# Kernel optimization log

Hardware: AMD Instinct MI355X
Metric: run time of the kernel (lower is better)

## Reference

```python
import jax, jax.numpy as jnp
import numpy as np

D_MODEL = 2048
N_HEADS = 16
HEAD_DIM = D_MODEL // N_HEADS
B, T = 2, 2048


def setup_inputs() -> dict:
    key = jax.random.key(0)
    ks = jax.random.split(key, 7)
    s = 0.02
    return {
        "x": jax.random.normal(ks[0], (B, T, D_MODEL), dtype=jnp.float32),
        "w_qkv": jax.random.normal(ks[1], (D_MODEL, 3 * D_MODEL), dtype=jnp.float32) * s,
        "w_proj": jax.random.normal(ks[2], (D_MODEL, D_MODEL), dtype=jnp.float32) * s,
        "w_ff1": jax.random.normal(ks[3], (D_MODEL, 4 * D_MODEL), dtype=jnp.float32) * s,
        "b_ff1": jnp.zeros((4 * D_MODEL,), dtype=jnp.float32),
        "w_ff2": jax.random.normal(ks[4], (4 * D_MODEL, D_MODEL), dtype=jnp.float32) * s,
        "b_ff2": jnp.zeros((D_MODEL,), dtype=jnp.float32),
    }


def reference(x, w_qkv, w_proj, w_ff1, b_ff1, w_ff2, b_ff2):
    Bs, Ts, C = x.shape
    H, hd = N_HEADS, HEAD_DIM
    # fused qkv projection
    qkv = jnp.einsum("btc,cd->btd", x, w_qkv)
    q, k, v = jnp.split(qkv, 3, axis=-1)
    # (B, T, C) -> (B, H, T, hd)
    q = q.reshape(Bs, Ts, H, hd).transpose(0, 2, 1, 3)
    k = k.reshape(Bs, Ts, H, hd).transpose(0, 2, 1, 3)
    v = v.reshape(Bs, Ts, H, hd).transpose(0, 2, 1, 3)
    # paged KV write + gather round-trip (empty cache, n_kv_head == n_heads)
    # is the identity on k, v; attention is causal SDPA over the full cache.
    scale = 1.0 / jnp.sqrt(jnp.asarray(hd, dtype=x.dtype))
    scores = jnp.einsum("bhqd,bhkd->bhqk", q, k) * scale
    causal = jnp.tril(jnp.ones((Ts, Ts), dtype=bool))
    scores = jnp.where(causal, scores, jnp.finfo(scores.dtype).min)
    attn = jax.nn.softmax(scores, axis=-1)
    out = jnp.einsum("bhqk,bhkd->bhqd", attn, v)  # (B, H, T, hd)
    out = out.transpose(0, 2, 1, 3).reshape(Bs, Ts, C)
    attn_out = jnp.einsum("btc,cd->btd", out, w_proj)
    # feed-forward with exact GELU (torch nn.GELU default)
    h = jax.nn.gelu(jnp.einsum("btc,cf->btf", x, w_ff1) + b_ff1, approximate=False)
    ff_out = jnp.einsum("btf,fc->btc", h, w_ff2) + b_ff2
    return x + attn_out + ff_out
```

## Files before the change

### kernel.cpp

```cpp
#include <hip/hip_runtime.h>
#include <hip/hip_bf16.h>
#include <cmath>

typedef __bf16 bf16x8 __attribute__((ext_vector_type(8)));
typedef float f32x4 __attribute__((ext_vector_type(4)));
typedef unsigned short u16;
typedef unsigned int u32;

#define DEV __device__ __forceinline__

static constexpr int BB = 2;
static constexpr int T = 2048;
static constexpr int DM = 2048;
static constexpr int NH = 16;
static constexpr int HD = 128;
static constexpr int FF = 8192;
static constexpr int M = BB * T;
static constexpr int NQKV = 3 * DM;

DEV u16 f2b(float f) {
  u32 u = __builtin_bit_cast(u32, f);
  u = (u + 0x7FFFu + ((u >> 16) & 1u)) >> 16;
  return (u16)u;
}
DEV float b2f(u16 h) {
  u32 u = ((u32)h) << 16;
  return __builtin_bit_cast(float, u);
}

DEV void gload16(const u16* g, const u16* l) {
  __builtin_amdgcn_global_load_lds(
      (const __attribute__((address_space(1))) void*)(uintptr_t)g,
      (__attribute__((address_space(3))) void*)(unsigned)(uintptr_t)l,
      16, 0, 0);
}


__global__ void cvt_f32_to_bf16(const float* __restrict__ in, u16* __restrict__ out, int n4) {
  int i = blockIdx.x * blockDim.x + threadIdx.x;
  if (i >= n4) return;
  float4 v = reinterpret_cast<const float4*>(in)[i];
  ushort4 o;
  o.x = f2b(v.x); o.y = f2b(v.y); o.z = f2b(v.z); o.w = f2b(v.w);
  reinterpret_cast<ushort4*>(out)[i] = o;
}

__global__ void transpose_cvt(const float* __restrict__ W, u16* __restrict__ Wt, int K, int N) {
  __shared__ float tile[32][33];
  int nb = blockIdx.x * 32, kb = blockIdx.y * 32;
  int r = threadIdx.x >> 3;
  int c4 = (threadIdx.x & 7) * 4;
  float4 v = *reinterpret_cast<const float4*>(&W[(size_t)(kb + r) * N + nb + c4]);
  tile[r][c4] = v.x; tile[r][c4 + 1] = v.y; tile[r][c4 + 2] = v.z; tile[r][c4 + 3] = v.w;
  __syncthreads();
  ushort4 o;
  o.x = f2b(tile[c4][r]);     o.y = f2b(tile[c4 + 1][r]);
  o.z = f2b(tile[c4 + 2][r]); o.w = f2b(tile[c4 + 3][r]);
  *reinterpret_cast<ushort4*>(&Wt[(size_t)(nb + r) * K + kb + c4]) = o;
}

template <int EPI>
__global__ __launch_bounds__(512, 2) void gemm8(
    const u16* __restrict__ A, const u16* __restrict__ Bt, int Ndim, int K, int gx,
    u16* __restrict__ out_bf, const float* __restrict__ bias) {
  __shared__ __align__(16) u16 lds[2 * 32768];
  const int t = threadIdx.x;
  const int nwg = gridDim.x, cpx = nwg >> 3;
  const int wg = (blockIdx.x & 7) * cpx + (blockIdx.x >> 3);
  const int m0 = (wg / gx) * 256, n0 = (wg % gx) * 256;
  const int wave = t >> 6, lane = t & 63;
  const int wm = wave >> 2, wn = wave & 3;
  const int lr = lane & 15, lk = lane >> 4;

  const int srow = t >> 3;
  const int sc8 = ((t & 7) ^ (srow & 7)) * 8;
  const u16* gA = &A[(size_t)(m0 + srow) * K + sc8];
  const u16* gB = &Bt[(size_t)(n0 + srow) * K + sc8];
  const int wls = wave * 512;

  u16* buf0 = lds;
  u16* buf1 = lds + 32768;

#define STAGE_A(buf, h, kt)                                                      \
  {                                                                              \
    gload16(gA + (size_t)((h) * 128) * K + (kt) * 64, (buf) + (h) * 8192 + wls); \
    gload16(gA + (size_t)((h) * 128 + 64) * K + (kt) * 64,                       \
            (buf) + (h) * 8192 + 4096 + wls);                                    \
  }
#define STAGE_B(buf, h, kt)                                                      \
  {                                                                              \
    gload16(gB + (size_t)((h) * 128) * K + (kt) * 64,                            \
            (buf) + 16384 + (h) * 8192 + wls);                                   \
    gload16(gB + (size_t)((h) * 128 + 64) * K + (kt) * 64,                       \
            (buf) + 16384 + (h) * 8192 + 4096 + wls);                            \
  }
#define PH_PRE                          \
  __builtin_amdgcn_sched_barrier(0);    \
  __builtin_amdgcn_s_barrier();         \
  __builtin_amdgcn_sched_barrier(0);    \
  __builtin_amdgcn_s_setprio(1);
#define PH_POST                         \
  __builtin_amdgcn_s_setprio(0);        \
  __builtin_amdgcn_sched_barrier(0);    \
  __builtin_amdgcn_s_barrier();         \
  __builtin_amdgcn_sched_barrier(0);

  const int NT = K >> 6;

  STAGE_A(buf0, 0, 0); STAGE_A(buf0, 1, 0);
  STAGE_B(buf0, 0, 0); STAGE_B(buf0, 1, 0);
  STAGE_A(buf1, 0, 1); STAGE_B(buf1, 0, 1);
  __builtin_amdgcn_sched_barrier(0);
  asm volatile("s_waitcnt vmcnt(4)" ::: "memory");
  __builtin_amdgcn_s_barrier();
  __builtin_amdgcn_sched_barrier(0);

  f32x4 acc[8][4] = {};
  const int aBase = (wm * 128 + lr) * 64;
  const int bBase = 16384 + (wn * 64 + lr) * 64;
  const int c0 = (lk ^ (lr & 7)) * 8;
  const int c1 = ((4 + lk) ^ (lr & 7)) * 8;

  u16* cur = buf0;
  u16* alt = buf1;
  bf16x8 af[4][2], bq0[2][2], bq1[2][2];

  for (int kt = 0; kt < NT; ++kt) {
#pragma unroll
    for (int i = 0; i < 4; ++i) {
      af[i][0] = *(const bf16x8*)&cur[aBase + i * 1024 + c0];
      af[i][1] = *(const bf16x8*)&cur[aBase + i * 1024 + c1];
    }
#pragma unroll
    for (int j = 0; j < 2; ++j) {
      bq0[j][0] = *(const bf16x8*)&cur[bBase + j * 1024 + c0];
      bq0[j][1] = *(const bf16x8*)&cur[bBase + j * 1024 + c1];
    }
    if (kt + 1 < NT) STAGE_A(alt, 1, kt + 1);
    PH_PRE;
#pragma unroll
    for (int i = 0; i < 4; ++i)
#pragma unroll
      for (int j = 0; j < 2; ++j)
#pragma unroll
        for (int kk = 0; kk < 2; ++kk)
          acc[i][j] = __builtin_amdgcn_mfma_f32_16x16x32_bf16(af[i][kk], bq0[j][kk], acc[i][j], 0, 0, 0);
    PH_POST;
#pragma unroll
    for (int j = 0; j < 2; ++j) {
      bq1[j][0] = *(const bf16x8*)&cur[bBase + (2 + j) * 1024 + c0];
      bq1[j][1] = *(const bf16x8*)&cur[bBase + (2 + j) * 1024 + c1];
    }
    if (kt + 1 < NT) STAGE_B(alt, 1, kt + 1);
    PH_PRE;
#pragma unroll
    for (int i = 0; i < 4; ++i)
#pragma unroll
      for (int j = 0; j < 2; ++j)
#pragma unroll
        for (int kk = 0; kk < 2; ++kk)
          acc[i][2 + j] = __builtin_amdgcn_mfma_f32_16x16x32_bf16(af[i][kk], bq1[j][kk], acc[i][2 + j], 0, 0, 0);
    PH_POST;
#pragma unroll
    for (int i = 0; i < 4; ++i) {
      af[i][0] = *(const bf16x8*)&cur[aBase + (4 + i) * 1024 + c0];
      af[i][1] = *(const bf16x8*)&cur[aBase + (4 + i) * 1024 + c1];
    }
    if (kt + 2 < NT) STAGE_A(cur, 0, kt + 2);
    PH_PRE;
#pragma unroll
    for (int i = 0; i < 4; ++i)
#pragma unroll
      for (int j = 0; j < 2; ++j)
#pragma unroll
        for (int kk = 0; kk < 2; ++kk)
          acc[4 + i][2 + j] = __builtin_amdgcn_mfma_f32_16x16x32_bf16(af[i][kk], bq1[j][kk], acc[4 + i][2 + j], 0, 0, 0);
    PH_POST;
    if (kt + 2 < NT) STAGE_B(cur, 0, kt + 2);
    PH_PRE;
#pragma unroll
    for (int i = 0; i < 4; ++i)
#pragma unroll
      for (int j = 0; j < 2; ++j)
#pragma unroll
        for (int kk = 0; kk < 2; ++kk)
          acc[4 + i][j] = __builtin_amdgcn_mfma_f32_16x16x32_bf16(af[i][kk], bq0[j][kk], acc[4 + i][j], 0, 0, 0);
    __builtin_amdgcn_s_setprio(0);
    __builtin_amdgcn_sched_barrier(0);
    if (kt + 2 < NT)      asm volatile("s_waitcnt vmcnt(4)" ::: "memory");
    else if (kt + 1 < NT) asm volatile("s_waitcnt vmcnt(0)" ::: "memory");
    __builtin_amdgcn_s_barrier();
    __builtin_amdgcn_sched_barrier(0);
    u16* tmp = cur; cur = alt; alt = tmp;
  }
#undef STAGE_A
#undef STAGE_B
#undef PH_PRE
#undef PH_POST

#pragma unroll
  for (int i = 0; i < 8; ++i) {
#pragma unroll
    for (int j = 0; j < 4; ++j) {
#pragma unroll
      for (int r = 0; r < 4; ++r) {
        int gr = m0 + wm * 128 + i * 16 + (lane >> 4) * 4 + r;
        int gc = n0 + wn * 64 + j * 16 + (lane & 15);
        float v = acc[i][j][r];
        if constexpr (EPI == 0) {
          int part = gc >> 11, cc = gc & 2047;
          int head = cc >> 7, d = cc & 127;
          int b = gr >> 11, tt = gr & 2047;
          out_bf[(size_t)part * M * DM + (((size_t)(b * NH + head) * T + tt) * HD + d)] = f2b(v);
        } else {
          v += bias[gc];
          float u = v * (v * v * 0.044715f + 1.0f) * 0.7978845608028654f;
          float e = exp2f(u * 2.885390081777927f);
          float th = 1.0f - 2.0f / (e + 1.0f);
          v = 0.5f * v * (1.0f + th);
          out_bf[(size_t)gr * Ndim + gc] = f2b(v);
        }
      }
    }
  }
}

template <int EPI>
__global__ __launch_bounds__(512, 4) void gemm_bf16(
    const u16* __restrict__ A, const u16* __restrict__ Bt, int Ndim, int K, int gx,
    u16* __restrict__ out_bf, float* __restrict__ out_f32,
    const float* __restrict__ bias,
    const float* __restrict__ resid_f32, const u16* __restrict__ resid_bf) {
  __shared__ __align__(16) u16 lds[3 * (256 + 128) * 32];
  const int t = threadIdx.x;
  const int nwg = gridDim.x, cpx = nwg >> 3;
  const int wg = (blockIdx.x & 7) * cpx + (blockIdx.x >> 3);
  const int m0 = (wg / gx) * 256, n0 = (wg % gx) * 128;
  const int wave = t >> 6, lane = t & 63;
  const int wm = wave >> 1, wn = wave & 1;
  const int lr = lane & 15, lk = lane >> 4;

  u16* cA = lds;                   u16* cB = lds + 8192;
  u16* nA = lds + 12288;           u16* nB = lds + 12288 + 8192;
  u16* sA = lds + 2 * 12288;       u16* sB = lds + 2 * 12288 + 8192;

  const int sk = ((lane & 3) ^ ((lane >> 3) & 3)) * 8;
  const u16* gA0 = &A[(size_t)(m0 + wave * 16 + (lane >> 2)) * K + sk];
  const u16* gA1 = gA0 + (size_t)128 * K;
  const u16* gB0 = &Bt[(size_t)(n0 + wave * 16 + (lane >> 2)) * K + sk];

  const int wbase = wave * 512;

  auto stage = [&](u16* dA, u16* dB) {
    gload16(gA0, dA + wbase);
    gload16(gA1, dA + 4096 + wbase);
    gload16(gB0, dB + wbase);
    gA0 += 32; gA1 += 32; gB0 += 32;
  };

  const int NT = K >> 5;

  stage(cA, cB);
  stage(nA, nB);
  __builtin_amdgcn_sched_barrier(0);
  asm volatile("s_waitcnt vmcnt(3)" ::: "memory");
  __builtin_amdgcn_s_barrier();
  __builtin_amdgcn_sched_barrier(0);

  f32x4 acc[4][4] = {};
  const int rcol = (lk ^ ((lr >> 1) & 3)) * 8;

  for (int kt = 0; kt < NT; ++kt) {
    if (kt + 2 < NT) stage(sA, sB);
    bf16x8 af[4], bfr[4];
#pragma unroll
    for (int i = 0; i < 4; ++i) {
      af[i]  = *reinterpret_cast<const bf16x8*>(&cA[(wm * 64 + i * 16 + lr) * 32 + rcol]);
      bfr[i] = *reinterpret_cast<const bf16x8*>(&cB[(wn * 64 + i * 16 + lr) * 32 + rcol]);
    }
#pragma unroll
    for (int i = 0; i < 4; ++i)
#pragma unroll
      for (int j = 0; j < 4; ++j)
        acc[i][j] = __builtin_amdgcn_mfma_f32_16x16x32_bf16(af[i], bfr[j], acc[i][j], 0, 0, 0);
    if (kt + 1 < NT) {
      __builtin_amdgcn_sched_barrier(0);
      if (kt + 2 < NT) asm volatile("s_waitcnt vmcnt(3)" ::: "memory");
      else             asm volatile("s_waitcnt vmcnt(0)" ::: "memory");
      __builtin_amdgcn_s_barrier();
      __builtin_amdgcn_sched_barrier(0);
      u16* tA = cA; u16* tB = cB;
      cA = nA; cB = nB; nA = sA; nB = sB; sA = tA; sB = tB;
    }
  }

#pragma unroll
  for (int i = 0; i < 4; ++i) {
#pragma unroll
    for (int j = 0; j < 4; ++j) {
#pragma unroll
      for (int r = 0; r < 4; ++r) {
        int gr = m0 + wm * 64 + i * 16 + (lane >> 4) * 4 + r;
        int gc = n0 + wn * 64 + j * 16 + (lane & 15);
        float v = acc[i][j][r];
        if constexpr (EPI == 1) {
          out_bf[(size_t)gr * Ndim + gc] = f2b(v);
        } else if constexpr (EPI == 3) {
          v += bias[gc] + resid_f32[(size_t)gr * Ndim + gc] + b2f(resid_bf[(size_t)gr * Ndim + gc]);
          out_f32[(size_t)gr * Ndim + gc] = v;
        } else {
          int hh = gr >> 7, d = gr & 127;
          int b = gc >> 11, tt = gc & 2047;
          out_bf[((size_t)(b * NH + hh) * HD + d) * T + tt] = f2b(v);
        }
      }
    }
  }
}

__global__ __launch_bounds__(512) void attn_fwd(
    const u16* __restrict__ qg, const u16* __restrict__ kg,
    const u16* __restrict__ vt, u16* __restrict__ outg) {
  __shared__ __align__(16) u16 lK[64 * 128];
  __shared__ __align__(16) u16 lVt[128 * 64];
  __shared__ __align__(16) u16 lP[8][16 * 72];
  const int t = threadIdx.x;
  const int qi = gridDim.x - 1 - blockIdx.x;
  const int bh = blockIdx.y;
  const int wv = t >> 6, lane = t & 63;
  const int lc = lane & 15, lg = lane >> 4;
  const size_t base = (size_t)bh * T * HD;
  const size_t vbase = (size_t)bh * HD * T;
  const int q0 = qi * 128;

  bf16x8 qf[4];
#pragma unroll
  for (int kk = 0; kk < 4; ++kk)
    qf[kk] = *reinterpret_cast<const bf16x8*>(
        &qg[base + (size_t)(q0 + wv * 16 + lc) * HD + kk * 32 + lg * 8]);

  f32x4 oacc[8] = {};
  float mrow[4], lrow[4];
#pragma unroll
  for (int r = 0; r < 4; ++r) { mrow[r] = -INFINITY; lrow[r] = 0.f; }

  const float scaleL = 0.08838834764831845f * 1.4426950408889634f;
  const int ntiles = 2 * qi + 2;
  for (int kt = 0; kt < ntiles; ++kt) {
    __syncthreads();
#pragma unroll
    for (int h = 0; h < 2; ++h) {
      int c = t + h * 512;
      int row = c >> 4;
      int sb = ((c & 15) * 16) ^ ((row & 7) << 4);
      gload16(&kg[base + (size_t)(kt * 64 + row) * HD + (sb >> 1)],
              (const u16*)((const char*)lK + ((h * 8 + wv) * 64) * 16));
    }
#pragma unroll
    for (int h = 0; h < 2; ++h) {
      int c = t + h * 512;
      int row = c >> 3;
      int sb = ((c & 7) * 16) ^ ((row & 7) << 4);
      gload16(&vt[vbase + (size_t)row * T + kt * 64 + (sb >> 1)],
              (const u16*)((const char*)lVt + ((h * 8 + wv) * 64) * 16));
    }
    __syncthreads();

    f32x4 s[4] = {};
    __builtin_amdgcn_s_setprio(1);
#pragma unroll
    for (int nf = 0; nf < 4; ++nf) {
      int krow = nf * 16 + lc;
#pragma unroll
      for (int kk = 0; kk < 4; ++kk) {
        int dbyte = kk * 64 + lg * 16;
        bf16x8 kf = *reinterpret_cast<const bf16x8*>(
            reinterpret_cast<const char*>(lK) + krow * 256 + (dbyte ^ ((krow & 7) << 4)));
        s[nf] = __builtin_amdgcn_mfma_f32_16x16x32_bf16(qf[kk], kf, s[nf], 0, 0, 0);
      }
    }
    __builtin_amdgcn_s_setprio(0);

    float rmax[4];
#pragma unroll
    for (int r = 0; r < 4; ++r) rmax[r] = -INFINITY;
#pragma unroll
    for (int nf = 0; nf < 4; ++nf) {
      int col = kt * 64 + nf * 16 + lc;
#pragma unroll
      for (int r = 0; r < 4; ++r) {
        int row = q0 + wv * 16 + lg * 4 + r;
        float sv = s[nf][r] * scaleL;
        if (col > row) sv = -INFINITY;
        s[nf][r] = sv;
        rmax[r] = fmaxf(rmax[r], sv);
      }
    }
#pragma unroll
    for (int mk = 1; mk < 16; mk <<= 1)
#pragma unroll
      for (int r = 0; r < 4; ++r)
        rmax[r] = fmaxf(rmax[r], __shfl_xor(rmax[r], mk));

    int need = 0;
#pragma unroll
    for (int r = 0; r < 4; ++r) need |= (rmax[r] > mrow[r] + 11.5f) ? 1 : 0;
    if (__any(need)) {
      float corr[4];
#pragma unroll
      for (int r = 0; r < 4; ++r) {
        float mnew = fmaxf(mrow[r], rmax[r]);
        corr[r] = exp2f(mrow[r] - mnew);
        mrow[r] = mnew;
        lrow[r] *= corr[r];
      }
#pragma unroll
      for (int dc = 0; dc < 8; ++dc)
#pragma unroll
        for (int r = 0; r < 4; ++r) oacc[dc][r] *= corr[r];
    }

#pragma unroll
    for (int nf = 0; nf < 4; ++nf) {
#pragma unroll
      for (int r = 0; r < 4; ++r) {
        float p = exp2f(s[nf][r] - mrow[r]);
        lrow[r] += p;
        lP[wv][(lg * 4 + r) * 72 + nf * 16 + lc] = f2b(p);
      }
    }
    bf16x8 pa[2];
#pragma unroll
    for (int kk = 0; kk < 2; ++kk)
      pa[kk] = *reinterpret_cast<const bf16x8*>(&lP[wv][lc * 72 + kk * 32 + lg * 8]);
    __builtin_amdgcn_s_setprio(1);
#pragma unroll
    for (int dc = 0; dc < 8; ++dc) {
#pragma unroll
      for (int kk = 0; kk < 2; ++kk) {
        int vrow = dc * 16 + lc;
        int off = (kk * 64 + lg * 16) ^ ((vrow & 7) << 4);
        bf16x8 vf = *reinterpret_cast<const bf16x8*>(
            reinterpret_cast<const char*>(lVt) + vrow * 128 + off);
        oacc[dc] = __builtin_amdgcn_mfma_f32_16x16x32_bf16(pa[kk], vf, oacc[dc], 0, 0, 0);
      }
    }
    __builtin_amdgcn_s_setprio(0);
  }

#pragma unroll
  for (int mk = 1; mk < 16; mk <<= 1)
#pragma unroll
    for (int r = 0; r < 4; ++r) lrow[r] += __shfl_xor(lrow[r], mk);

  const int b = bh >> 4, hh = bh & 15;
#pragma unroll
  for (int dc = 0; dc < 8; ++dc)
#pragma unroll
    for (int r = 0; r < 4; ++r) {
      int tt = q0 + wv * 16 + lg * 4 + r;
      int d = dc * 16 + lc;
      float o = oacc[dc][r] / lrow[r];
      outg[(size_t)(b * T + tt) * DM + hh * HD + d] = f2b(o);
    }
}


extern "C" void kernel_launch(void* const* d_in, const int* in_sizes, int n_in,
                              void* d_out, int out_size, void* d_ws, size_t ws_size,
                              hipStream_t stream) {
  const float* x      = (const float*)d_in[0];
  const float* w_qkv  = (const float*)d_in[1];
  const float* w_proj = (const float*)d_in[2];
  const float* w_ff1  = (const float*)d_in[3];
  const float* b_ff1  = (const float*)d_in[4];
  const float* w_ff2  = (const float*)d_in[5];
  const float* b_ff2  = (const float*)d_in[6];
  float* out = (float*)d_out;

  u16* ws = (u16*)d_ws;
  size_t o = 0;
  u16* x_bf      = ws + o; o += (size_t)M * DM;
  u16* wqkv_t    = ws + o; o += (size_t)NQKV * DM;
  u16* wproj_t   = ws + o; o += (size_t)DM * DM;
  u16* wff1_t    = ws + o; o += (size_t)FF * DM;
  u16* wff2_t    = ws + o; o += (size_t)DM * FF;
  u16* attn_proj = ws + o; o += (size_t)M * DM;
  u16* qbuf      = ws + o;
  u16* kbuf      = qbuf + (size_t)M * DM;
  u16* vtbuf     = kbuf + (size_t)M * DM;
  u16* attn_out  = vtbuf + (size_t)M * DM;
  u16* hbuf      = qbuf;

  cvt_f32_to_bf16<<<(M * DM / 4 + 255) / 256, 256, 0, stream>>>(x, x_bf, M * DM / 4);
  transpose_cvt<<<dim3(NQKV / 32, DM / 32), 256, 0, stream>>>(w_qkv, wqkv_t, DM, NQKV);
  transpose_cvt<<<dim3(DM / 32, DM / 32), 256, 0, stream>>>(w_proj, wproj_t, DM, DM);
  transpose_cvt<<<dim3(FF / 32, DM / 32), 256, 0, stream>>>(w_ff1, wff1_t, DM, FF);
  transpose_cvt<<<dim3(DM / 32, FF / 32), 256, 0, stream>>>(w_ff2, wff2_t, FF, DM);

  gemm8<0><<<256, 512, 0, stream>>>(x_bf, wqkv_t, 4096, DM, 16, qbuf, nullptr);

  gemm_bf16<4><<<256, 512, 0, stream>>>(
      wqkv_t + (size_t)4096 * DM, x_bf, M, DM, 32, vtbuf, nullptr, nullptr, nullptr, nullptr);

  attn_fwd<<<dim3(T / 128, BB * NH), 512, 0, stream>>>(qbuf, kbuf, vtbuf, attn_out);

  gemm_bf16<1><<<256, 512, 0, stream>>>(
      attn_out, wproj_t, DM, DM, 16, attn_proj, nullptr, nullptr, nullptr, nullptr);

  gemm8<2><<<512, 512, 0, stream>>>(x_bf, wff1_t, FF, DM, 32, hbuf, b_ff1);

  gemm_bf16<3><<<256, 512, 0, stream>>>(
      hbuf, wff2_t, DM, FF, 16, nullptr, out, b_ff2, x, attn_proj);
}
```

Before: 668.2 us.

## Double-buffer K/V tiles in attention and shrink query block to 64 rows

The attention kernel now uses 256-thread blocks covering 64 query rows each, which doubles the grid. K and V tiles are double-buffered in LDS: the next tile is prefetched while the current one is being computed, with one barrier per iteration instead of two. The aim is to hide global-to-LDS load latency behind MFMA work and to balance the causal workload across more, smaller blocks. The trade-off is that each K/V tile is now reloaded by twice as many blocks, and each block uses more LDS, which may limit occupancy.

```diff
diff --git a/kernel.cpp b/kernel.cpp
--- a/kernel.cpp
+++ b/kernel.cpp
@@ -318,12 +318,12 @@
   }
 }
 
-__global__ __launch_bounds__(512) void attn_fwd(
+__global__ __launch_bounds__(256) void attn_fwd(
     const u16* __restrict__ qg, const u16* __restrict__ kg,
     const u16* __restrict__ vt, u16* __restrict__ outg) {
-  __shared__ __align__(16) u16 lK[64 * 128];
-  __shared__ __align__(16) u16 lVt[128 * 64];
-  __shared__ __align__(16) u16 lP[8][16 * 72];
+  __shared__ __align__(16) u16 lK[2][64 * 128];
+  __shared__ __align__(16) u16 lVt[2][128 * 64];
+  __shared__ __align__(16) u16 lP[4][16 * 72];
   const int t = threadIdx.x;
   const int qi = gridDim.x - 1 - blockIdx.x;
   const int bh = blockIdx.y;
@@ -331,7 +331,7 @@
   const int lc = lane & 15, lg = lane >> 4;
   const size_t base = (size_t)bh * T * HD;
   const size_t vbase = (size_t)bh * HD * T;
-  const int q0 = qi * 128;
+  const int q0 = qi * 64;
 
   bf16x8 qf[4];
 #pragma unroll
@@ -344,27 +344,39 @@
 #pragma unroll
   for (int r = 0; r < 4; ++r) { mrow[r] = -INFINITY; lrow[r] = 0.f; }
 
-  const float scaleL = 0.08838834764831845f * 1.4426950408889634f;
-  const int ntiles = 2 * qi + 2;
-  for (int kt = 0; kt < ntiles; ++kt) {
-    __syncthreads();
-#pragma unroll
-    for (int h = 0; h < 2; ++h) {
-      int c = t + h * 512;
+  auto stageKV = [&](int kt, int b) {
+#pragma unroll
+    for (int h = 0; h < 4; ++h) {
+      int c = t + h * 256;
       int row = c >> 4;
       int sb = ((c & 15) * 16) ^ ((row & 7) << 4);
       gload16(&kg[base + (size_t)(kt * 64 + row) * HD + (sb >> 1)],
-              (const u16*)((const char*)lK + ((h * 8 + wv) * 64) * 16));
-    }
-#pragma unroll
-    for (int h = 0; h < 2; ++h) {
-      int c = t + h * 512;
+              (const u16*)((const char*)lK[b] + (h * 256 + wv * 64) * 16));
+    }
+#pragma unroll
+    for (int h = 0; h < 4; ++h) {
+      int c = t + h * 256;
       int row = c >> 3;
       int sb = ((c & 7) * 16) ^ ((row & 7) << 4);
       gload16(&vt[vbase + (size_t)row * T + kt * 64 + (sb >> 1)],
-              (const u16*)((const char*)lVt + ((h * 8 + wv) * 64) * 16));
-    }
-    __syncthreads();
+              (const u16*)((const char*)lVt[b] + (h * 256 + wv * 64) * 16));
+    }
+  };
+
+  const float scaleL = 0.08838834764831845f * 1.4426950408889634f;
+  const int ntiles = qi + 1;
+
+  stageKV(0, 0);
+  __builtin_amdgcn_sched_barrier(0);
+  asm volatile("s_waitcnt vmcnt(0)" ::: "memory");
+  __builtin_amdgcn_s_barrier();
+  __builtin_amdgcn_sched_barrier(0);
+
+  for (int kt = 0; kt < ntiles; ++kt) {
+    const int cb = kt & 1;
+    if (kt + 1 < ntiles) stageKV(kt + 1, cb ^ 1);
+    const u16* lKc = lK[cb];
+    const u16* lVc = lVt[cb];
 
     f32x4 s[4] = {};
     __builtin_amdgcn_s_setprio(1);
@@ -375,7 +387,7 @@
       for (int kk = 0; kk < 4; ++kk) {
         int dbyte = kk * 64 + lg * 16;
         bf16x8 kf = *reinterpret_cast<const bf16x8*>(
-            reinterpret_cast<const char*>(lK) + krow * 256 + (dbyte ^ ((krow & 7) << 4)));
+            reinterpret_cast<const char*>(lKc) + krow * 256 + (dbyte ^ ((krow & 7) << 4)));
         s[nf] = __builtin_amdgcn_mfma_f32_16x16x32_bf16(qf[kk], kf, s[nf], 0, 0, 0);
       }
     }
@@ -441,11 +453,16 @@
         int vrow = dc * 16 + lc;
         int off = (kk * 64 + lg * 16) ^ ((vrow & 7) << 4);
         bf16x8 vf = *reinterpret_cast<const bf16x8*>(
-            reinterpret_cast<const char*>(lVt) + vrow * 128 + off);
+            reinterpret_cast<const char*>(lVc) + vrow * 128 + off);
         oacc[dc] = __builtin_amdgcn_mfma_f32_16x16x32_bf16(pa[kk], vf, oacc[dc], 0, 0, 0);
       }
     }
     __builtin_amdgcn_s_setprio(0);
+
+    __builtin_amdgcn_sched_barrier(0);
+    if (kt + 1 < ntiles) asm volatile("s_waitcnt vmcnt(0)" ::: "memory");
+    __builtin_amdgcn_s_barrier();
+    __builtin_amdgcn_sched_barrier(0);
   }
 
 #pragma unroll
@@ -503,7 +520,7 @@
   gemm_bf16<4><<<256, 512, 0, stream>>>(
       wqkv_t + (size_t)4096 * DM, x_bf, M, DM, 32, vtbuf, nullptr, nullptr, nullptr, nullptr);
 
-  attn_fwd<<<dim3(T / 128, BB * NH), 512, 0, stream>>>(qbuf, kbuf, vtbuf, attn_out);
+  attn_fwd<<<dim3(T / 64, BB * NH), 256, 0, stream>>>(qbuf, kbuf, vtbuf, attn_out);
 
   gemm_bf16<1><<<256, 512, 0, stream>>>(
       attn_out, wproj_t, DM, DM, 16, attn_proj, nullptr, nullptr, nullptr, nullptr);
```

After: 659.1 us. About the same (-1.4%).
